# Kernel optimization log

Hardware: AMD Instinct MI355X
Metric: run time of the kernel (lower is better)

The kernel has to match this reference:

```python
import jax, jax.numpy as jnp
import numpy as np

N = 199968   # active voxels (flat tokens)
W = 3125     # number of windows
S = 64       # window capacity
D = 128      # d_model
H = 8        # nhead
DH = D // H
DFF = 256


def layer_norm(x, g, b, eps=1e-5):
    m = x.mean(-1, keepdims=True)
    v = ((x - m) ** 2).mean(-1, keepdims=True)
    return (x - m) / jnp.sqrt(v + eps) * g + b


def setup_inputs() -> dict:
    key = jax.random.key(0)
    ks = jax.random.split(key, 12)
    s = 0.02
    src = jax.random.normal(ks[0], (N, D), dtype=jnp.float32)
    pos = jax.random.normal(ks[1], (W, S, D), dtype=jnp.float32)
    # token i occupies flat window-slot i; slots >= N are padding
    inds = jnp.arange(N, dtype=jnp.int64)
    key_padding_mask = (jnp.arange(W * S) >= N).reshape(W, S)  # True = pad
    in_proj_w = jax.random.normal(ks[2], (3 * D, D), dtype=jnp.float32) * s
    in_proj_b = jax.random.normal(ks[3], (3 * D,), dtype=jnp.float32) * s
    out_w = jax.random.normal(ks[4], (D, D), dtype=jnp.float32) * s
    out_b = jax.random.normal(ks[5], (D,), dtype=jnp.float32) * s
    w1 = jax.random.normal(ks[6], (DFF, D), dtype=jnp.float32) * s
    b1 = jax.random.normal(ks[7], (DFF,), dtype=jnp.float32) * s
    w2 = jax.random.normal(ks[8], (D, DFF), dtype=jnp.float32) * s
    b2 = jax.random.normal(ks[9], (D,), dtype=jnp.float32) * s
    ln1_g = jnp.ones((D,), jnp.float32); ln1_b = jnp.zeros((D,), jnp.float32)
    ln2_g = jnp.ones((D,), jnp.float32); ln2_b = jnp.zeros((D,), jnp.float32)
    return {"src": src, "pos": pos, "inds": inds,
            "key_padding_mask": key_padding_mask,
            "in_proj_w": in_proj_w, "in_proj_b": in_proj_b,
            "out_w": out_w, "out_b": out_b,
            "w1": w1, "b1": b1, "w2": w2, "b2": b2,
            "ln1_g": ln1_g, "ln1_b": ln1_b, "ln2_g": ln2_g, "ln2_b": ln2_b}


def reference(src, pos, inds, key_padding_mask, in_proj_w, in_proj_b,
              out_w, out_b, w1, b1, w2, b2, ln1_g, ln1_b, ln2_g, ln2_b):
    # ---- flat2window_v2: scatter flat tokens into window slots ----
    win = jnp.zeros((W * S, D), src.dtype).at[inds].set(src).reshape(W, S, D)
    # q = k = feat + pos, v = feat (post-norm, self-attention branch)
    qk_in = win + pos
    Wq, Wk, Wv = in_proj_w[:D], in_proj_w[D:2 * D], in_proj_w[2 * D:]
    bq, bk, bv = in_proj_b[:D], in_proj_b[D:2 * D], in_proj_b[2 * D:]
    q = (qk_in @ Wq.T + bq).reshape(W, S, H, DH)
    k = (qk_in @ Wk.T + bk).reshape(W, S, H, DH)
    v = (win @ Wv.T + bv).reshape(W, S, H, DH)
    scale = 1.0 / jnp.sqrt(jnp.asarray(DH, src.dtype))
    scores = jnp.einsum('wqhd,wkhd->whqk', q, k) * scale  # [W,H,S,S]
    scores = jnp.where(key_padding_mask[:, None, None, :], -jnp.inf, scores)
    attn = jax.nn.softmax(scores, axis=-1)
    o = jnp.einsum('whqk,wkhd->wqhd', attn, v).reshape(W, S, D)
    o = o @ out_w.T + out_b
    # ---- window2flat_v2: gather back to flat tokens ----
    att_out = o.reshape(W * S, D)[inds]
    # ---- residual + LN + FFN + LN (post_norm=True, dropout=0 eval) ----
    x = layer_norm(src + att_out, ln1_g, ln1_b)
    ffn = jax.nn.relu(x @ w1.T + b1) @ w2.T + b2
    x = layer_norm(x + ffn, ln2_g, ln2_b)
    return x
```

## Files before the change

### kernel.cpp

```cpp
#include <hip/hip_runtime.h>
#include <stdint.h>

typedef __attribute__((ext_vector_type(8))) short bf16x8;
typedef __attribute__((ext_vector_type(4))) float f32x4;
typedef __attribute__((ext_vector_type(16))) float f32x16;

#define MFMA16(a,b,c) __builtin_amdgcn_mfma_f32_16x16x32_bf16((a),(b),(c),0,0,0)
#define MFMA32(a,b,c) __builtin_amdgcn_mfma_f32_32x32x16_bf16((a),(b),(c),0,0,0)

#define RA 0
#define RB 16384
#define RC 32768
#define RED 49152
#define LDSB (49152 + 2048)
#define QSCALE 0.36067376022224085f

static __device__ __forceinline__ int swz16(int row, int byte){ return byte ^ ((row&15)<<4); }
static __device__ __forceinline__ int swz8 (int row, int byte){ return byte ^ ((row&7)<<4); }

static __device__ __forceinline__ void barrier_lds(){
  asm volatile("s_waitcnt lgkmcnt(0)" ::: "memory");
  __builtin_amdgcn_s_barrier();
}

static __device__ __forceinline__ uint32_t cvtpk(float lo, float hi){
  uint32_t r; asm("v_cvt_pk_bf16_f32 %0, %1, %2" : "=v"(r) : "v"(lo), "v"(hi)); return r;
}
static __device__ __forceinline__ unsigned short f2bf(float f){
  union { float f; uint32_t u; } c; c.f = f;
  return (unsigned short)((c.u + 0x7fffu + ((c.u >> 16) & 1u)) >> 16);
}
static __device__ __forceinline__ f32x16 zero16(){
  f32x16 z;
  #pragma unroll
  for (int e=0;e<16;++e) z[e]=0.f;
  return z;
}

static __device__ __forceinline__ void packPT(const f32x16 s, int hi, bf16x8& fA, bf16x8& fB){
  uint32_t PA0=cvtpk(s[0],s[1]),  PA1=cvtpk(s[2],s[3]);
  uint32_t PB0=cvtpk(s[4],s[5]),  PB1=cvtpk(s[6],s[7]);
  uint32_t PC0=cvtpk(s[8],s[9]),  PC1=cvtpk(s[10],s[11]);
  uint32_t PD0=cvtpk(s[12],s[13]),PD1=cvtpk(s[14],s[15]);
  uint32_t x0 = __shfl_xor(hi ? PA0 : PB0, 32);
  uint32_t x1 = __shfl_xor(hi ? PA1 : PB1, 32);
  uint32_t y0 = __shfl_xor(hi ? PC0 : PD0, 32);
  uint32_t y1 = __shfl_xor(hi ? PC1 : PD1, 32);
  union { uint32_t u[4]; bf16x8 v; } ua, ub;
  ua.u[0] = hi ? x0 : PA0;  ua.u[1] = hi ? x1 : PA1;
  ua.u[2] = hi ? PB0 : x0;  ua.u[3] = hi ? PB1 : x1;
  ub.u[0] = hi ? y0 : PC0;  ub.u[1] = hi ? y1 : PC1;
  ub.u[2] = hi ? PD0 : y0;  ub.u[3] = hi ? PD1 : y1;
  fA = ua.v; fB = ub.v;
}

__global__ void convert_weights(const float* __restrict__ ipw, const float* __restrict__ ow,
                                const float* __restrict__ w1, const float* __restrict__ w2,
                                unsigned short* __restrict__ wsb){
  int i = blockIdx.x*256 + threadIdx.x;
  if (i >= 131072) return;
  const float* sp; int m, K, KC;
  if (i < 49152)      { sp = ipw; m = i;         K=128; KC=4; }
  else if (i < 65536) { sp = ow;  m = i - 49152; K=128; KC=4; }
  else if (i < 98304) { sp = w1;  m = i - 65536; K=128; KC=4; }
  else                { sp = w2;  m = i - 98304; K=256; KC=8; }
  int e  = m & 7;
  int L  = (m >> 3) & 63;
  int b  = m >> 9;
  int kc = b % KC;
  int Mt = b / KC;
  float v = sp[(Mt*16 + (L&15))*K + kc*32 + (L>>4)*8 + e];
  if (i < 16384) v *= QSCALE;
  wsb[i] = f2bf(v);
}

__global__ __launch_bounds__(256, 3) void enc_kernel(
    const float* __restrict__ src, const float* __restrict__ pos,
    const float* __restrict__ ipb, const float* __restrict__ obp,
    const float* __restrict__ b1p, const float* __restrict__ b2p,
    const float* __restrict__ g1p, const float* __restrict__ be1p,
    const float* __restrict__ g2p, const float* __restrict__ be2p,
    const unsigned short* __restrict__ wb,
    float* __restrict__ out, int nTok)
{
  __shared__ __align__(16) char sm[LDSB];
  const int win  = blockIdx.x;
  const int tid  = threadIdx.x;
  const int lane = tid & 63;
  const int wid  = tid >> 6;
  const int l15  = lane & 15;
  const int lg   = lane >> 4;
  const int l31  = lane & 31;
  const int hi   = lane >> 5;
  const f32x4 FZ = {0.f,0.f,0.f,0.f};
  const int colbase = wid*32;
  const unsigned short* wlane = wb + lane*8;
  const int valid = nTok - win*64;

  f32x4 srcv[2][4];
  #pragma unroll
  for (int Mtl=0;Mtl<2;++Mtl){
    #pragma unroll
    for (int g=0;g<4;++g){
      int row  = g*16 + l15;
      int grow = win*64 + row;
      int col  = colbase + Mtl*16 + lg*4;
      f32x4 sv = FZ;
      if (grow < nTok) sv = *(const f32x4*)(src + (size_t)grow*128 + col);
      f32x4 pv = *(const f32x4*)(pos + (size_t)win*8192 + row*128 + col);
      srcv[Mtl][g] = sv;
      uint2 wv, qv;
      wv.x = cvtpk(sv[0], sv[1]);             wv.y = cvtpk(sv[2], sv[3]);
      qv.x = cvtpk(sv[0]+pv[0], sv[1]+pv[1]); qv.y = cvtpk(sv[2]+pv[2], sv[3]+pv[3]);
      int cb = col*2;
      *(uint2*)(sm + RA + row*256 + swz16(row, cb)) = qv;
      *(uint2*)(sm + RB + row*256 + swz16(row, cb)) = wv;
    }
  }
  barrier_lds();

  {
    {
      bf16x8 wv8[8];
      #pragma unroll
      for (int i=0;i<8;++i)
        wv8[i] = *(const bf16x8*)(wlane + (size_t)(((16 + wid*2 + (i>>2))*4 + (i&3)) << 9));
      f32x4 vacc[2][4];
      #pragma unroll
      for (int Mtl=0;Mtl<2;++Mtl){
        #pragma unroll
        for (int g=0;g<4;++g) vacc[Mtl][g] = FZ;
      }
      #pragma unroll
      for (int kc=0;kc<4;++kc){
        bf16x8 aw[4];
        #pragma unroll
        for (int g=0;g<4;++g){
          int r2 = g*16 + l15;
          aw[g] = *(const bf16x8*)(sm + RB + r2*256 + swz16(r2, kc*64 + lg*16));
        }
        #pragma unroll
        for (int Mtl=0;Mtl<2;++Mtl){
          #pragma unroll
          for (int g=0;g<4;++g) vacc[Mtl][g] = MFMA16(aw[g], wv8[Mtl*4+kc], vacc[Mtl][g]);
        }
      }
      #pragma unroll
      for (int Mtl=0;Mtl<2;++Mtl){
        int d = colbase + Mtl*16 + l15;
        float bv = ipb[256 + d];
        #pragma unroll
        for (int g=0;g<4;++g){
          uint2 vp;
          vp.x = cvtpk(vacc[Mtl][g][0]+bv, vacc[Mtl][g][1]+bv);
          vp.y = cvtpk(vacc[Mtl][g][2]+bv, vacc[Mtl][g][3]+bv);
          *(uint2*)(sm + RC + d*128 + swz8(d, (g*16 + lg*4)*2)) = vp;
        }
      }
    }

    f32x4 qacc[2][4];
    {
      bf16x8 wq8[8];
      #pragma unroll
      for (int i=0;i<8;++i)
        wq8[i] = *(const bf16x8*)(wlane + (size_t)((( 0 + wid*2 + (i>>2))*4 + (i&3)) << 9));
      #pragma unroll
      for (int Mtl=0;Mtl<2;++Mtl){
        #pragma unroll
        for (int g=0;g<4;++g) qacc[Mtl][g]=FZ;
      }
      #pragma unroll
      for (int kc=0;kc<4;++kc){
        bf16x8 bq[4];
        #pragma unroll
        for (int g=0;g<4;++g){
          int r2 = g*16 + l15;
          bq[g] = *(const bf16x8*)(sm + RA + r2*256 + swz16(r2, kc*64 + lg*16));
        }
        #pragma unroll
        for (int Mtl=0;Mtl<2;++Mtl){
          #pragma unroll
          for (int g=0;g<4;++g) qacc[Mtl][g] = MFMA16(wq8[Mtl*4+kc], bq[g], qacc[Mtl][g]);
        }
      }
    }
    barrier_lds();

    #pragma unroll
    for (int Mtl=0;Mtl<2;++Mtl){
      f32x4 qb4 = *(const f32x4*)(ipb + colbase + Mtl*16 + lg*4);
      #pragma unroll
      for (int g=0;g<4;++g){
        int tok = g*16 + l15;
        int cb  = (colbase + Mtl*16 + lg*4)*2;
        uint2 qp;
        qp.x = cvtpk(qacc[Mtl][g][0]+qb4[0]*QSCALE, qacc[Mtl][g][1]+qb4[1]*QSCALE);
        qp.y = cvtpk(qacc[Mtl][g][2]+qb4[2]*QSCALE, qacc[Mtl][g][3]+qb4[3]*QSCALE);
        *(uint2*)(sm + RB + tok*256 + swz16(tok, cb)) = qp;
      }
    }

    f32x4 kacc[2][4];
    {
      bf16x8 wk8[8];
      #pragma unroll
      for (int i=0;i<8;++i)
        wk8[i] = *(const bf16x8*)(wlane + (size_t)((( 8 + wid*2 + (i>>2))*4 + (i&3)) << 9));
      #pragma unroll
      for (int Mtl=0;Mtl<2;++Mtl){
        #pragma unroll
        for (int g=0;g<4;++g) kacc[Mtl][g]=FZ;
      }
      #pragma unroll
      for (int kc=0;kc<4;++kc){
        bf16x8 bq[4];
        #pragma unroll
        for (int g=0;g<4;++g){
          int r2 = g*16 + l15;
          bq[g] = *(const bf16x8*)(sm + RA + r2*256 + swz16(r2, kc*64 + lg*16));
        }
        #pragma unroll
        for (int Mtl=0;Mtl<2;++Mtl){
          #pragma unroll
          for (int g=0;g<4;++g) kacc[Mtl][g] = MFMA16(wk8[Mtl*4+kc], bq[g], kacc[Mtl][g]);
        }
      }
    }
    barrier_lds();

    #pragma unroll
    for (int Mtl=0;Mtl<2;++Mtl){
      f32x4 kb4 = *(const f32x4*)(ipb + 128 + colbase + Mtl*16 + lg*4);
      #pragma unroll
      for (int g=0;g<4;++g){
        int tok = g*16 + l15;
        int cb  = (colbase + Mtl*16 + lg*4)*2;
        uint2 kp;
        kp.x = cvtpk(kacc[Mtl][g][0]+kb4[0], kacc[Mtl][g][1]+kb4[1]);
        kp.y = cvtpk(kacc[Mtl][g][2]+kb4[2], kacc[Mtl][g][3]+kb4[3]);
        *(uint2*)(sm + RA + tok*256 + swz16(tok, cb)) = kp;
      }
    }
  }

  #pragma unroll
  for (int hh=0; hh<2; ++hh){
    const int head = wid*2 + hh;
    bf16x8 ka0 = *(const bf16x8*)(sm + RA + (     l31)*256 + swz16(l31,    head*32 + hi*16));
    bf16x8 ka1 = *(const bf16x8*)(sm + RA + (32 + l31)*256 + swz16(32+l31, head*32 + hi*16));
    #pragma unroll
    for (int qt=0; qt<2; ++qt){
      int qrow = qt*32 + l31;
      bf16x8 qb = *(const bf16x8*)(sm + RB + qrow*256 + swz16(qrow, head*32 + hi*16));
      f32x16 s0 = MFMA32(ka0, qb, zero16());
      f32x16 s1 = MFMA32(ka1, qb, zero16());
      if (valid < 64){
        #pragma unroll
        for (int e=0;e<16;++e){
          int kk = (e&3) + 8*(e>>2) + 4*hi;
          if (kk      >= valid) s0[e] = -1e30f;
          if (kk + 32 >= valid) s1[e] = -1e30f;
        }
      }
      #pragma unroll
      for (int e=0;e<16;++e) s0[e] = __builtin_amdgcn_exp2f(s0[e]);
      #pragma unroll
      for (int e=0;e<16;++e) s1[e] = __builtin_amdgcn_exp2f(s1[e]);
      float t[8];
      #pragma unroll
      for (int e=0;e<8;++e) t[e] = (s0[2*e]+s0[2*e+1]) + (s1[2*e]+s1[2*e+1]);
      float u0 = t[0]+t[1], u1 = t[2]+t[3], u2 = t[4]+t[5], u3 = t[6]+t[7];
      float sum = (u0+u1)+(u2+u3);
      sum += __shfl_xor(sum, 32);
      float rden = __builtin_amdgcn_rcpf(sum);

      bf16x8 fr[4];
      packPT(s0, hi, fr[0], fr[1]);
      packPT(s1, hi, fr[2], fr[3]);
      f32x16 oacc = zero16();
      #pragma unroll
      for (int kc=0;kc<4;++kc){
        int vrow = head*16 + l15;
        bf16x8 va = *(const bf16x8*)(sm + RC + vrow*128 + swz8(vrow, kc*32 + hi*16));
        oacc = MFMA32(va, fr[kc], oacc);
      }
      int tok = qt*32 + l31;
      uint2 o01, o23;
      o01.x = cvtpk(oacc[0]*rden, oacc[1]*rden);
      o01.y = cvtpk(oacc[2]*rden, oacc[3]*rden);
      o23.x = cvtpk(oacc[4]*rden, oacc[5]*rden);
      o23.y = cvtpk(oacc[6]*rden, oacc[7]*rden);
      *(uint2*)(sm + RB + tok*256 + swz16(tok, (head*16 + 4*hi)*2))     = o01;
      *(uint2*)(sm + RB + tok*256 + swz16(tok, (head*16 + 8 + 4*hi)*2)) = o23;
    }
  }
  barrier_lds();

  f32x4 xva[2][4];
  {
    bf16x8 wo8[8];
    #pragma unroll
    for (int i=0;i<8;++i)
      wo8[i] = *(const bf16x8*)(wlane + 49152 + (size_t)(((wid*2 + (i>>2))*4 + (i&3)) << 9));
    f32x4 oa[2][4];
    #pragma unroll
    for (int Mtl=0;Mtl<2;++Mtl){
      #pragma unroll
      for (int g=0;g<4;++g) oa[Mtl][g] = FZ;
    }
    #pragma unroll
    for (int kc=0;kc<4;++kc){
      bf16x8 bo[4];
      #pragma unroll
      for (int g=0;g<4;++g){
        int r2 = g*16 + l15;
        bo[g] = *(const bf16x8*)(sm + RB + r2*256 + swz16(r2, kc*64 + lg*16));
      }
      #pragma unroll
      for (int Mtl=0;Mtl<2;++Mtl){
        #pragma unroll
        for (int g=0;g<4;++g) oa[Mtl][g] = MFMA16(wo8[Mtl*4+kc], bo[g], oa[Mtl][g]);
      }
    }
    #pragma unroll
    for (int Mtl=0;Mtl<2;++Mtl){
      f32x4 ob4 = *(const f32x4*)(obp + colbase + Mtl*16 + lg*4);
      #pragma unroll
      for (int g=0;g<4;++g){
        #pragma unroll
        for (int r=0;r<4;++r) xva[Mtl][g][r] = oa[Mtl][g][r] + ob4[r] + srcv[Mtl][g][r];
      }
    }
    float* redc = (float*)(sm + RED);
    #pragma unroll
    for (int g=0;g<4;++g){
      float ts=0.f, tq=0.f;
      #pragma unroll
      for (int Mtl=0;Mtl<2;++Mtl){
        #pragma unroll
        for (int r=0;r<4;++r){ float v = xva[Mtl][g][r]; ts += v; tq += v*v; }
      }
      ts += __shfl_xor(ts,16); tq += __shfl_xor(tq,16);
      ts += __shfl_xor(ts,32); tq += __shfl_xor(tq,32);
      if (lg == 0) *(float2*)(redc + (g*16+l15)*8 + wid*2) = make_float2(ts, tq);
    }
    barrier_lds();
    float mean4[4], rstd4[4];
    #pragma unroll
    for (int g=0;g<4;++g){
      int tok = g*16 + l15;
      f32x4 ra = *(const f32x4*)(redc + tok*8);
      f32x4 rb = *(const f32x4*)(redc + tok*8 + 4);
      float sum = ra[0]+ra[2]+rb[0]+rb[2];
      float sq  = ra[1]+ra[3]+rb[1]+rb[3];
      mean4[g] = sum*(1.f/128.f);
      rstd4[g] = __builtin_amdgcn_rsqf(sq*(1.f/128.f) - mean4[g]*mean4[g] + 1e-5f);
    }
    #pragma unroll
    for (int Mtl=0;Mtl<2;++Mtl){
      f32x4 g4 = *(const f32x4*)(g1p  + colbase + Mtl*16 + lg*4);
      f32x4 e4 = *(const f32x4*)(be1p + colbase + Mtl*16 + lg*4);
      #pragma unroll
      for (int g=0;g<4;++g){
        int tok = g*16 + l15;
        int cb  = (colbase + Mtl*16 + lg*4)*2;
        #pragma unroll
        for (int r=0;r<4;++r) xva[Mtl][g][r] = (xva[Mtl][g][r]-mean4[g])*rstd4[g]*g4[r] + e4[r];
        uint2 xp;
        xp.x = cvtpk(xva[Mtl][g][0], xva[Mtl][g][1]);
        xp.y = cvtpk(xva[Mtl][g][2], xva[Mtl][g][3]);
        *(uint2*)(sm + RA + tok*256 + swz16(tok, cb)) = xp;
      }
    }
  }
  barrier_lds();

  {
    char* hreg = (wid < 2) ? (sm + RB) : (sm + RC);
    int   hoff = (wid & 1)*64;
    #pragma unroll 1
    for (int half=0; half<2; ++half){
      bf16x8 wf[8];
      #pragma unroll
      for (int i=0;i<8;++i)
        wf[i] = *(const bf16x8*)(wlane + 65536 + (size_t)(((wid*4 + half*2 + (i>>2))*4 + (i&3)) << 9));
      f32x4 ha[2][4];
      #pragma unroll
      for (int Mtl=0;Mtl<2;++Mtl){
        #pragma unroll
        for (int g=0;g<4;++g) ha[Mtl][g] = FZ;
      }
      #pragma unroll
      for (int kc=0;kc<4;++kc){
        bf16x8 bx[4];
        #pragma unroll
        for (int g=0;g<4;++g){
          int r2 = g*16 + l15;
          bx[g] = *(const bf16x8*)(sm + RA + r2*256 + swz16(r2, kc*64 + lg*16));
        }
        #pragma unroll
        for (int Mtl=0;Mtl<2;++Mtl){
          #pragma unroll
          for (int g=0;g<4;++g) ha[Mtl][g] = MFMA16(wf[Mtl*4+kc], bx[g], ha[Mtl][g]);
        }
      }
      #pragma unroll
      for (int Mtl=0;Mtl<2;++Mtl){
        int Mg = half*2 + Mtl;
        f32x4 b14 = *(const f32x4*)(b1p + wid*64 + Mg*16 + lg*4);
        #pragma unroll
        for (int g=0;g<4;++g){
          int tok = g*16 + l15;
          float h0 = fmaxf(ha[Mtl][g][0]+b14[0], 0.f);
          float h1 = fmaxf(ha[Mtl][g][1]+b14[1], 0.f);
          float h2 = fmaxf(ha[Mtl][g][2]+b14[2], 0.f);
          float h3 = fmaxf(ha[Mtl][g][3]+b14[3], 0.f);
          int cb = (hoff + Mg*16 + lg*4)*2;
          uint2 hp;
          hp.x = cvtpk(h0, h1);
          hp.y = cvtpk(h2, h3);
          *(uint2*)(hreg + tok*256 + swz16(tok, cb)) = hp;
        }
      }
    }
  }
  barrier_lds();

  {
    f32x4 fa[2][4];
    #pragma unroll
    for (int Mtl=0;Mtl<2;++Mtl){
      #pragma unroll
      for (int g=0;g<4;++g) fa[Mtl][g] = FZ;
    }
    #pragma unroll 1
    for (int half=0; half<2; ++half){
      bf16x8 wg[8];
      #pragma unroll
      for (int i=0;i<8;++i)
        wg[i] = *(const bf16x8*)(wlane + 98304 + (size_t)(((wid*2 + (i>>2))*8 + half*4 + (i&3)) << 9));
      const char* hsrc = sm + (half ? RC : RB);
      #pragma unroll
      for (int kc=0;kc<4;++kc){
        bf16x8 bh[4];
        #pragma unroll
        for (int g=0;g<4;++g){
          int r2 = g*16 + l15;
          bh[g] = *(const bf16x8*)(hsrc + r2*256 + swz16(r2, kc*64 + lg*16));
        }
        #pragma unroll
        for (int Mtl=0;Mtl<2;++Mtl){
          #pragma unroll
          for (int g=0;g<4;++g) fa[Mtl][g] = MFMA16(wg[Mtl*4+kc], bh[g], fa[Mtl][g]);
        }
      }
    }
    #pragma unroll
    for (int Mtl=0;Mtl<2;++Mtl){
      f32x4 b24 = *(const f32x4*)(b2p + colbase + Mtl*16 + lg*4);
      #pragma unroll
      for (int g=0;g<4;++g){
        #pragma unroll
        for (int r=0;r<4;++r) fa[Mtl][g][r] += b24[r] + xva[Mtl][g][r];
      }
    }
    float* redc = (float*)(sm + RED);
    #pragma unroll
    for (int g=0;g<4;++g){
      float ts=0.f, tq=0.f;
      #pragma unroll
      for (int Mtl=0;Mtl<2;++Mtl){
        #pragma unroll
        for (int r=0;r<4;++r){ float v = fa[Mtl][g][r]; ts += v; tq += v*v; }
      }
      ts += __shfl_xor(ts,16); tq += __shfl_xor(tq,16);
      ts += __shfl_xor(ts,32); tq += __shfl_xor(tq,32);
      if (lg == 0) *(float2*)(redc + (g*16+l15)*8 + wid*2) = make_float2(ts, tq);
    }
    barrier_lds();
    float m2[4], r2v[4];
    #pragma unroll
    for (int g=0;g<4;++g){
      int tok = g*16 + l15;
      f32x4 ra = *(const f32x4*)(redc + tok*8);
      f32x4 rb = *(const f32x4*)(redc + tok*8 + 4);
      float sum = ra[0]+ra[2]+rb[0]+rb[2];
      float sq  = ra[1]+ra[3]+rb[1]+rb[3];
      m2[g]  = sum*(1.f/128.f);
      r2v[g] = __builtin_amdgcn_rsqf(sq*(1.f/128.f) - m2[g]*m2[g] + 1e-5f);
    }
    #pragma unroll
    for (int Mtl=0;Mtl<2;++Mtl){
      f32x4 g4 = *(const f32x4*)(g2p  + colbase + Mtl*16 + lg*4);
      f32x4 e4 = *(const f32x4*)(be2p + colbase + Mtl*16 + lg*4);
      #pragma unroll
      for (int g=0;g<4;++g){
        int tok = g*16 + l15;
        f32x4 o4;
        #pragma unroll
        for (int r=0;r<4;++r) o4[r] = (fa[Mtl][g][r]-m2[g])*r2v[g]*g4[r] + e4[r];
        int X = ((colbase + Mtl*16 + lg*4)*4) ^ (l15<<4);
        *(f32x4*)(sm + ((tok<32)? RA : RB) + (tok&31)*512 + X) = o4;
      }
    }
    barrier_lds();
    #pragma unroll
    for (int j=0;j<8;++j){
      int row  = wid*16 + j*2 + hi;
      int grow = win*64 + row;
      if (grow < nTok){
        int X = (l31*16) ^ ((row&15)<<4);
        f32x4 v = *(const f32x4*)(sm + ((row<32)? RA : RB) + (row&31)*512 + X);
        *(f32x4*)(out + (size_t)grow*128 + l31*4) = v;
      }
    }
  }
}

extern "C" void kernel_launch(void* const* d_in, const int* in_sizes, int n_in,
                              void* d_out, int out_size, void* d_ws, size_t ws_size,
                              hipStream_t stream) {
  const float* src = (const float*)d_in[0];
  const float* pos = (const float*)d_in[1];
  const float* ipw = (const float*)d_in[4];
  const float* ipb = (const float*)d_in[5];
  const float* ow  = (const float*)d_in[6];
  const float* ob  = (const float*)d_in[7];
  const float* w1  = (const float*)d_in[8];
  const float* b1  = (const float*)d_in[9];
  const float* w2  = (const float*)d_in[10];
  const float* b2  = (const float*)d_in[11];
  const float* g1  = (const float*)d_in[12];
  const float* be1 = (const float*)d_in[13];
  const float* g2  = (const float*)d_in[14];
  const float* be2 = (const float*)d_in[15];
  int nTok = in_sizes[0] / 128;
  int nWin = in_sizes[1] / 8192;
  unsigned short* wsb = (unsigned short*)d_ws;

  hipLaunchKernelGGL(convert_weights, dim3(512), dim3(256), 0, stream, ipw, ow, w1, w2, wsb);
  hipLaunchKernelGGL(enc_kernel, dim3(nWin), dim3(256), 0, stream,
                     src, pos, ipb, ob, b1, b2, g1, be1, g2, be2, wsb,
                     (float*)d_out, nTok);
}
```

Before: 139.9 us.

## Split per-window work across 8 waves instead of 4

The block grows from 256 to 512 threads, so each wave owns 16 output columns and one attention head rather than 32 columns and two heads. This halves the per-wave accumulator and weight-register arrays, raising the launch-bounds occupancy target from 3 to 4 blocks per CU. The LayerNorm reduction scratch is widened to hold eight partial sums per token, and the FFN hidden-layer write offsets are remapped to match. More waves per window add barrier contention, and each wave reuses its LDS operand loads across fewer MFMAs.

```diff
diff --git a/kernel.cpp b/kernel.cpp
--- a/kernel.cpp
+++ b/kernel.cpp
@@ -12,7 +12,7 @@
 #define RB 16384
 #define RC 32768
 #define RED 49152
-#define LDSB (49152 + 2048)
+#define LDSB (49152 + 4096)
 #define QSCALE 0.36067376022224085f
 
 static __device__ __forceinline__ int swz16(int row, int byte){ return byte ^ ((row&15)<<4); }
@@ -74,7 +74,7 @@
   wsb[i] = f2bf(v);
 }
 
-__global__ __launch_bounds__(256, 3) void enc_kernel(
+__global__ __launch_bounds__(512, 4) void enc_kernel(
     const float* __restrict__ src, const float* __restrict__ pos,
     const float* __restrict__ ipb, const float* __restrict__ obp,
     const float* __restrict__ b1p, const float* __restrict__ b2p,
@@ -93,44 +93,38 @@
   const int l31  = lane & 31;
   const int hi   = lane >> 5;
   const f32x4 FZ = {0.f,0.f,0.f,0.f};
-  const int colbase = wid*32;
+  const int colbase = wid*16;
   const unsigned short* wlane = wb + lane*8;
   const int valid = nTok - win*64;
 
-  f32x4 srcv[2][4];
+  f32x4 srcv[4];
   #pragma unroll
-  for (int Mtl=0;Mtl<2;++Mtl){
-    #pragma unroll
-    for (int g=0;g<4;++g){
-      int row  = g*16 + l15;
-      int grow = win*64 + row;
-      int col  = colbase + Mtl*16 + lg*4;
-      f32x4 sv = FZ;
-      if (grow < nTok) sv = *(const f32x4*)(src + (size_t)grow*128 + col);
-      f32x4 pv = *(const f32x4*)(pos + (size_t)win*8192 + row*128 + col);
-      srcv[Mtl][g] = sv;
-      uint2 wv, qv;
-      wv.x = cvtpk(sv[0], sv[1]);             wv.y = cvtpk(sv[2], sv[3]);
-      qv.x = cvtpk(sv[0]+pv[0], sv[1]+pv[1]); qv.y = cvtpk(sv[2]+pv[2], sv[3]+pv[3]);
-      int cb = col*2;
-      *(uint2*)(sm + RA + row*256 + swz16(row, cb)) = qv;
-      *(uint2*)(sm + RB + row*256 + swz16(row, cb)) = wv;
-    }
+  for (int g=0;g<4;++g){
+    int row  = g*16 + l15;
+    int grow = win*64 + row;
+    int col  = colbase + lg*4;
+    f32x4 sv = FZ;
+    if (grow < nTok) sv = *(const f32x4*)(src + (size_t)grow*128 + col);
+    f32x4 pv = *(const f32x4*)(pos + (size_t)win*8192 + row*128 + col);
+    srcv[g] = sv;
+    uint2 wv, qv;
+    wv.x = cvtpk(sv[0], sv[1]);             wv.y = cvtpk(sv[2], sv[3]);
+    qv.x = cvtpk(sv[0]+pv[0], sv[1]+pv[1]); qv.y = cvtpk(sv[2]+pv[2], sv[3]+pv[3]);
+    int cb = col*2;
+    *(uint2*)(sm + RA + row*256 + swz16(row, cb)) = qv;
+    *(uint2*)(sm + RB + row*256 + swz16(row, cb)) = wv;
   }
   barrier_lds();
 
   {
     {
-      bf16x8 wv8[8];
-      #pragma unroll
-      for (int i=0;i<8;++i)
-        wv8[i] = *(const bf16x8*)(wlane + (size_t)(((16 + wid*2 + (i>>2))*4 + (i&3)) << 9));
-      f32x4 vacc[2][4];
-      #pragma unroll
-      for (int Mtl=0;Mtl<2;++Mtl){
-        #pragma unroll
-        for (int g=0;g<4;++g) vacc[Mtl][g] = FZ;
-      }
+      bf16x8 wv8[4];
+      #pragma unroll
+      for (int kc=0;kc<4;++kc)
+        wv8[kc] = *(const bf16x8*)(wlane + (size_t)(((16 + wid)*4 + kc) << 9));
+      f32x4 vacc[4];
+      #pragma unroll
+      for (int g=0;g<4;++g) vacc[g] = FZ;
       #pragma unroll
       for (int kc=0;kc<4;++kc){
         bf16x8 aw[4];
@@ -140,36 +134,27 @@
           aw[g] = *(const bf16x8*)(sm + RB + r2*256 + swz16(r2, kc*64 + lg*16));
         }
         #pragma unroll
-        for (int Mtl=0;Mtl<2;++Mtl){
-          #pragma unroll
-          for (int g=0;g<4;++g) vacc[Mtl][g] = MFMA16(aw[g], wv8[Mtl*4+kc], vacc[Mtl][g]);
-        }
-      }
-      #pragma unroll
-      for (int Mtl=0;Mtl<2;++Mtl){
-        int d = colbase + Mtl*16 + l15;
-        float bv = ipb[256 + d];
-        #pragma unroll
-        for (int g=0;g<4;++g){
-          uint2 vp;
-          vp.x = cvtpk(vacc[Mtl][g][0]+bv, vacc[Mtl][g][1]+bv);
-          vp.y = cvtpk(vacc[Mtl][g][2]+bv, vacc[Mtl][g][3]+bv);
-          *(uint2*)(sm + RC + d*128 + swz8(d, (g*16 + lg*4)*2)) = vp;
-        }
-      }
-    }
-
-    f32x4 qacc[2][4];
+        for (int g=0;g<4;++g) vacc[g] = MFMA16(aw[g], wv8[kc], vacc[g]);
+      }
+      int d = colbase + l15;
+      float bv = ipb[256 + d];
+      #pragma unroll
+      for (int g=0;g<4;++g){
+        uint2 vp;
+        vp.x = cvtpk(vacc[g][0]+bv, vacc[g][1]+bv);
+        vp.y = cvtpk(vacc[g][2]+bv, vacc[g][3]+bv);
+        *(uint2*)(sm + RC + d*128 + swz8(d, (g*16 + lg*4)*2)) = vp;
+      }
+    }
+
+    f32x4 qacc[4];
     {
-      bf16x8 wq8[8];
-      #pragma unroll
-      for (int i=0;i<8;++i)
-        wq8[i] = *(const bf16x8*)(wlane + (size_t)((( 0 + wid*2 + (i>>2))*4 + (i&3)) << 9));
-      #pragma unroll
-      for (int Mtl=0;Mtl<2;++Mtl){
-        #pragma unroll
-        for (int g=0;g<4;++g) qacc[Mtl][g]=FZ;
-      }
+      bf16x8 wq8[4];
+      #pragma unroll
+      for (int kc=0;kc<4;++kc)
+        wq8[kc] = *(const bf16x8*)(wlane + (size_t)((wid*4 + kc) << 9));
+      #pragma unroll
+      for (int g=0;g<4;++g) qacc[g]=FZ;
       #pragma unroll
       for (int kc=0;kc<4;++kc){
         bf16x8 bq[4];
@@ -179,39 +164,32 @@
           bq[g] = *(const bf16x8*)(sm + RA + r2*256 + swz16(r2, kc*64 + lg*16));
         }
         #pragma unroll
-        for (int Mtl=0;Mtl<2;++Mtl){
-          #pragma unroll
-          for (int g=0;g<4;++g) qacc[Mtl][g] = MFMA16(wq8[Mtl*4+kc], bq[g], qacc[Mtl][g]);
-        }
+        for (int g=0;g<4;++g) qacc[g] = MFMA16(wq8[kc], bq[g], qacc[g]);
       }
     }
     barrier_lds();
 
-    #pragma unroll
-    for (int Mtl=0;Mtl<2;++Mtl){
-      f32x4 qb4 = *(const f32x4*)(ipb + colbase + Mtl*16 + lg*4);
+    {
+      f32x4 qb4 = *(const f32x4*)(ipb + colbase + lg*4);
       #pragma unroll
       for (int g=0;g<4;++g){
         int tok = g*16 + l15;
-        int cb  = (colbase + Mtl*16 + lg*4)*2;
+        int cb  = (colbase + lg*4)*2;
         uint2 qp;
-        qp.x = cvtpk(qacc[Mtl][g][0]+qb4[0]*QSCALE, qacc[Mtl][g][1]+qb4[1]*QSCALE);
-        qp.y = cvtpk(qacc[Mtl][g][2]+qb4[2]*QSCALE, qacc[Mtl][g][3]+qb4[3]*QSCALE);
+        qp.x = cvtpk(qacc[g][0]+qb4[0]*QSCALE, qacc[g][1]+qb4[1]*QSCALE);
+        qp.y = cvtpk(qacc[g][2]+qb4[2]*QSCALE, qacc[g][3]+qb4[3]*QSCALE);
         *(uint2*)(sm + RB + tok*256 + swz16(tok, cb)) = qp;
       }
     }
 
-    f32x4 kacc[2][4];
+    f32x4 kacc[4];
     {
-      bf16x8 wk8[8];
-      #pragma unroll
-      for (int i=0;i<8;++i)
-        wk8[i] = *(const bf16x8*)(wlane + (size_t)((( 8 + wid*2 + (i>>2))*4 + (i&3)) << 9));
-      #pragma unroll
-      for (int Mtl=0;Mtl<2;++Mtl){
-        #pragma unroll
-        for (int g=0;g<4;++g) kacc[Mtl][g]=FZ;
-      }
+      bf16x8 wk8[4];
+      #pragma unroll
+      for (int kc=0;kc<4;++kc)
+        wk8[kc] = *(const bf16x8*)(wlane + (size_t)(((8 + wid)*4 + kc) << 9));
+      #pragma unroll
+      for (int g=0;g<4;++g) kacc[g]=FZ;
       #pragma unroll
       for (int kc=0;kc<4;++kc){
         bf16x8 bq[4];
@@ -221,32 +199,27 @@
           bq[g] = *(const bf16x8*)(sm + RA + r2*256 + swz16(r2, kc*64 + lg*16));
         }
         #pragma unroll
-        for (int Mtl=0;Mtl<2;++Mtl){
-          #pragma unroll
-          for (int g=0;g<4;++g) kacc[Mtl][g] = MFMA16(wk8[Mtl*4+kc], bq[g], kacc[Mtl][g]);
-        }
+        for (int g=0;g<4;++g) kacc[g] = MFMA16(wk8[kc], bq[g], kacc[g]);
       }
     }
     barrier_lds();
 
-    #pragma unroll
-    for (int Mtl=0;Mtl<2;++Mtl){
-      f32x4 kb4 = *(const f32x4*)(ipb + 128 + colbase + Mtl*16 + lg*4);
+    {
+      f32x4 kb4 = *(const f32x4*)(ipb + 128 + colbase + lg*4);
       #pragma unroll
       for (int g=0;g<4;++g){
         int tok = g*16 + l15;
-        int cb  = (colbase + Mtl*16 + lg*4)*2;
+        int cb  = (colbase + lg*4)*2;
         uint2 kp;
-        kp.x = cvtpk(kacc[Mtl][g][0]+kb4[0], kacc[Mtl][g][1]+kb4[1]);
-        kp.y = cvtpk(kacc[Mtl][g][2]+kb4[2], kacc[Mtl][g][3]+kb4[3]);
+        kp.x = cvtpk(kacc[g][0]+kb4[0], kacc[g][1]+kb4[1]);
+        kp.y = cvtpk(kacc[g][2]+kb4[2], kacc[g][3]+kb4[3]);
         *(uint2*)(sm + RA + tok*256 + swz16(tok, cb)) = kp;
       }
     }
   }
 
-  #pragma unroll
-  for (int hh=0; hh<2; ++hh){
-    const int head = wid*2 + hh;
+  {
+    const int head = wid;
     bf16x8 ka0 = *(const bf16x8*)(sm + RA + (     l31)*256 + swz16(l31,    head*32 + hi*16));
     bf16x8 ka1 = *(const bf16x8*)(sm + RA + (32 + l31)*256 + swz16(32+l31, head*32 + hi*16));
     #pragma unroll
@@ -297,18 +270,16 @@
   }
   barrier_lds();
 
-  f32x4 xva[2][4];
+  f32x4 xva[4];
+  float mean4[4], rstd4[4];
   {
-    bf16x8 wo8[8];
-    #pragma unroll
-    for (int i=0;i<8;++i)
-      wo8[i] = *(const bf16x8*)(wlane + 49152 + (size_t)(((wid*2 + (i>>2))*4 + (i&3)) << 9));
-    f32x4 oa[2][4];
-    #pragma unroll
-    for (int Mtl=0;Mtl<2;++Mtl){
-      #pragma unroll
-      for (int g=0;g<4;++g) oa[Mtl][g] = FZ;
-    }
+    bf16x8 wo8[4];
+    #pragma unroll
+    for (int kc=0;kc<4;++kc)
+      wo8[kc] = *(const bf16x8*)(wlane + 49152 + (size_t)((wid*4 + kc) << 9));
+    f32x4 oa[4];
+    #pragma unroll
+    for (int g=0;g<4;++g) oa[g] = FZ;
     #pragma unroll
     for (int kc=0;kc<4;++kc){
       bf16x8 bo[4];
@@ -318,79 +289,64 @@
         bo[g] = *(const bf16x8*)(sm + RB + r2*256 + swz16(r2, kc*64 + lg*16));
       }
       #pragma unroll
-      for (int Mtl=0;Mtl<2;++Mtl){
-        #pragma unroll
-        for (int g=0;g<4;++g) oa[Mtl][g] = MFMA16(wo8[Mtl*4+kc], bo[g], oa[Mtl][g]);
-      }
-    }
-    #pragma unroll
-    for (int Mtl=0;Mtl<2;++Mtl){
-      f32x4 ob4 = *(const f32x4*)(obp + colbase + Mtl*16 + lg*4);
-      #pragma unroll
-      for (int g=0;g<4;++g){
-        #pragma unroll
-        for (int r=0;r<4;++r) xva[Mtl][g][r] = oa[Mtl][g][r] + ob4[r] + srcv[Mtl][g][r];
-      }
+      for (int g=0;g<4;++g) oa[g] = MFMA16(wo8[kc], bo[g], oa[g]);
+    }
+    f32x4 ob4 = *(const f32x4*)(obp + colbase + lg*4);
+    #pragma unroll
+    for (int g=0;g<4;++g){
+      #pragma unroll
+      for (int r=0;r<4;++r) xva[g][r] = oa[g][r] + ob4[r] + srcv[g][r];
     }
     float* redc = (float*)(sm + RED);
     #pragma unroll
     for (int g=0;g<4;++g){
-      float ts=0.f, tq=0.f;
-      #pragma unroll
-      for (int Mtl=0;Mtl<2;++Mtl){
-        #pragma unroll
-        for (int r=0;r<4;++r){ float v = xva[Mtl][g][r]; ts += v; tq += v*v; }
-      }
+      float ts = xva[g][0]+xva[g][1]+xva[g][2]+xva[g][3];
+      float tq = xva[g][0]*xva[g][0]+xva[g][1]*xva[g][1]+xva[g][2]*xva[g][2]+xva[g][3]*xva[g][3];
       ts += __shfl_xor(ts,16); tq += __shfl_xor(tq,16);
       ts += __shfl_xor(ts,32); tq += __shfl_xor(tq,32);
-      if (lg == 0) *(float2*)(redc + (g*16+l15)*8 + wid*2) = make_float2(ts, tq);
+      if (lg == 0) *(float2*)(redc + (g*16+l15)*16 + wid*2) = make_float2(ts, tq);
     }
     barrier_lds();
-    float mean4[4], rstd4[4];
     #pragma unroll
     for (int g=0;g<4;++g){
       int tok = g*16 + l15;
-      f32x4 ra = *(const f32x4*)(redc + tok*8);
-      f32x4 rb = *(const f32x4*)(redc + tok*8 + 4);
-      float sum = ra[0]+ra[2]+rb[0]+rb[2];
-      float sq  = ra[1]+ra[3]+rb[1]+rb[3];
+      float sum=0.f, sq=0.f;
+      #pragma unroll
+      for (int c=0;c<4;++c){
+        f32x4 rr = *(const f32x4*)(redc + tok*16 + c*4);
+        sum += rr[0]+rr[2];
+        sq  += rr[1]+rr[3];
+      }
       mean4[g] = sum*(1.f/128.f);
       rstd4[g] = __builtin_amdgcn_rsqf(sq*(1.f/128.f) - mean4[g]*mean4[g] + 1e-5f);
     }
-    #pragma unroll
-    for (int Mtl=0;Mtl<2;++Mtl){
-      f32x4 g4 = *(const f32x4*)(g1p  + colbase + Mtl*16 + lg*4);
-      f32x4 e4 = *(const f32x4*)(be1p + colbase + Mtl*16 + lg*4);
-      #pragma unroll
-      for (int g=0;g<4;++g){
-        int tok = g*16 + l15;
-        int cb  = (colbase + Mtl*16 + lg*4)*2;
-        #pragma unroll
-        for (int r=0;r<4;++r) xva[Mtl][g][r] = (xva[Mtl][g][r]-mean4[g])*rstd4[g]*g4[r] + e4[r];
-        uint2 xp;
-        xp.x = cvtpk(xva[Mtl][g][0], xva[Mtl][g][1]);
-        xp.y = cvtpk(xva[Mtl][g][2], xva[Mtl][g][3]);
-        *(uint2*)(sm + RA + tok*256 + swz16(tok, cb)) = xp;
-      }
+    f32x4 g4 = *(const f32x4*)(g1p  + colbase + lg*4);
+    f32x4 e4 = *(const f32x4*)(be1p + colbase + lg*4);
+    #pragma unroll
+    for (int g=0;g<4;++g){
+      int tok = g*16 + l15;
+      int cb  = (colbase + lg*4)*2;
+      #pragma unroll
+      for (int r=0;r<4;++r) xva[g][r] = (xva[g][r]-mean4[g])*rstd4[g]*g4[r] + e4[r];
+      uint2 xp;
+      xp.x = cvtpk(xva[g][0], xva[g][1]);
+      xp.y = cvtpk(xva[g][2], xva[g][3]);
+      *(uint2*)(sm + RA + tok*256 + swz16(tok, cb)) = xp;
     }
   }
   barrier_lds();
 
   {
-    char* hreg = (wid < 2) ? (sm + RB) : (sm + RC);
-    int   hoff = (wid & 1)*64;
+    char* hreg = (wid < 4) ? (sm + RB) : (sm + RC);
     #pragma unroll 1
     for (int half=0; half<2; ++half){
-      bf16x8 wf[8];
-      #pragma unroll
-      for (int i=0;i<8;++i)
-        wf[i] = *(const bf16x8*)(wlane + 65536 + (size_t)(((wid*4 + half*2 + (i>>2))*4 + (i&3)) << 9));
-      f32x4 ha[2][4];
-      #pragma unroll
-      for (int Mtl=0;Mtl<2;++Mtl){
-        #pragma unroll
-        for (int g=0;g<4;++g) ha[Mtl][g] = FZ;
-      }
+      bf16x8 wf[4];
+      #pragma unroll
+      for (int kc=0;kc<4;++kc)
+        wf[kc] = *(const bf16x8*)(wlane + 65536 + (size_t)(((wid*2 + half)*4 + kc) << 9));
+      f32x4 ha[4];
+      #pragma unroll
+      for (int g=0;g<4;++g) ha[g] = FZ;
       #pragma unroll
       for (int kc=0;kc<4;++kc){
         bf16x8 bx[4];
@@ -400,114 +356,94 @@
           bx[g] = *(const bf16x8*)(sm + RA + r2*256 + swz16(r2, kc*64 + lg*16));
         }
         #pragma unroll
-        for (int Mtl=0;Mtl<2;++Mtl){
-          #pragma unroll
-          for (int g=0;g<4;++g) ha[Mtl][g] = MFMA16(wf[Mtl*4+kc], bx[g], ha[Mtl][g]);
-        }
-      }
-      #pragma unroll
-      for (int Mtl=0;Mtl<2;++Mtl){
-        int Mg = half*2 + Mtl;
-        f32x4 b14 = *(const f32x4*)(b1p + wid*64 + Mg*16 + lg*4);
-        #pragma unroll
-        for (int g=0;g<4;++g){
-          int tok = g*16 + l15;
-          float h0 = fmaxf(ha[Mtl][g][0]+b14[0], 0.f);
-          float h1 = fmaxf(ha[Mtl][g][1]+b14[1], 0.f);
-          float h2 = fmaxf(ha[Mtl][g][2]+b14[2], 0.f);
-          float h3 = fmaxf(ha[Mtl][g][3]+b14[3], 0.f);
-          int cb = (hoff + Mg*16 + lg*4)*2;
-          uint2 hp;
-          hp.x = cvtpk(h0, h1);
-          hp.y = cvtpk(h2, h3);
-          *(uint2*)(hreg + tok*256 + swz16(tok, cb)) = hp;
-        }
+        for (int g=0;g<4;++g) ha[g] = MFMA16(wf[kc], bx[g], ha[g]);
+      }
+      f32x4 b14 = *(const f32x4*)(b1p + (wid*2+half)*16 + lg*4);
+      #pragma unroll
+      for (int g=0;g<4;++g){
+        int tok = g*16 + l15;
+        float h0 = fmaxf(ha[g][0]+b14[0], 0.f);
+        float h1 = fmaxf(ha[g][1]+b14[1], 0.f);
+        float h2 = fmaxf(ha[g][2]+b14[2], 0.f);
+        float h3 = fmaxf(ha[g][3]+b14[3], 0.f);
+        int cb = ((wid&3)*32 + half*16 + lg*4)*2;
+        uint2 hp;
+        hp.x = cvtpk(h0, h1);
+        hp.y = cvtpk(h2, h3);
+        *(uint2*)(hreg + tok*256 + swz16(tok, cb)) = hp;
       }
     }
   }
   barrier_lds();
 
   {
-    f32x4 fa[2][4];
-    #pragma unroll
-    for (int Mtl=0;Mtl<2;++Mtl){
-      #pragma unroll
-      for (int g=0;g<4;++g) fa[Mtl][g] = FZ;
-    }
+    f32x4 fa[4];
+    #pragma unroll
+    for (int g=0;g<4;++g) fa[g] = FZ;
     #pragma unroll 1
     for (int half=0; half<2; ++half){
-      bf16x8 wg[8];
-      #pragma unroll
-      for (int i=0;i<8;++i)
-        wg[i] = *(const bf16x8*)(wlane + 98304 + (size_t)(((wid*2 + (i>>2))*8 + half*4 + (i&3)) << 9));
+      bf16x8 wg[4];
+      #pragma unroll
+      for (int kcl=0;kcl<4;++kcl)
+        wg[kcl] = *(const bf16x8*)(wlane + 98304 + (size_t)((wid*8 + half*4 + kcl) << 9));
       const char* hsrc = sm + (half ? RC : RB);
       #pragma unroll
-      for (int kc=0;kc<4;++kc){
+      for (int kcl=0;kcl<4;++kcl){
         bf16x8 bh[4];
         #pragma unroll
         for (int g=0;g<4;++g){
           int r2 = g*16 + l15;
-          bh[g] = *(const bf16x8*)(hsrc + r2*256 + swz16(r2, kc*64 + lg*16));
-        }
-        #pragma unroll
-        for (int Mtl=0;Mtl<2;++Mtl){
-          #pragma unroll
-          for (int g=0;g<4;++g) fa[Mtl][g] = MFMA16(wg[Mtl*4+kc], bh[g], fa[Mtl][g]);
-        }
-      }
-    }
-    #pragma unroll
-    for (int Mtl=0;Mtl<2;++Mtl){
-      f32x4 b24 = *(const f32x4*)(b2p + colbase + Mtl*16 + lg*4);
-      #pragma unroll
-      for (int g=0;g<4;++g){
-        #pragma unroll
-        for (int r=0;r<4;++r) fa[Mtl][g][r] += b24[r] + xva[Mtl][g][r];
-      }
+          bh[g] = *(const bf16x8*)(hsrc + r2*256 + swz16(r2, kcl*64 + lg*16));
+        }
+        #pragma unroll
+        for (int g=0;g<4;++g) fa[g] = MFMA16(wg[kcl], bh[g], fa[g]);
+      }
+    }
+    f32x4 b24 = *(const f32x4*)(b2p + colbase + lg*4);
+    #pragma unroll
+    for (int g=0;g<4;++g){
+      #pragma unroll
+      for (int r=0;r<4;++r) fa[g][r] += b24[r] + xva[g][r];
     }
     float* redc = (float*)(sm + RED);
     #pragma unroll
     for (int g=0;g<4;++g){
-      float ts=0.f, tq=0.f;
-      #pragma unroll
-      for (int Mtl=0;Mtl<2;++Mtl){
-        #pragma unroll
-        for (int r=0;r<4;++r){ float v = fa[Mtl][g][r]; ts += v; tq += v*v; }
-      }
+      float ts = fa[g][0]+fa[g][1]+fa[g][2]+fa[g][3];
+      float tq = fa[g][0]*fa[g][0]+fa[g][1]*fa[g][1]+fa[g][2]*fa[g][2]+fa[g][3]*fa[g][3];
       ts += __shfl_xor(ts,16); tq += __shfl_xor(tq,16);
       ts += __shfl_xor(ts,32); tq += __shfl_xor(tq,32);
-      if (lg == 0) *(float2*)(redc + (g*16+l15)*8 + wid*2) = make_float2(ts, tq);
+      if (lg == 0) *(float2*)(redc + (g*16+l15)*16 + wid*2) = make_float2(ts, tq);
     }
     barrier_lds();
     float m2[4], r2v[4];
     #pragma unroll
     for (int g=0;g<4;++g){
       int tok = g*16 + l15;
-      f32x4 ra = *(const f32x4*)(redc + tok*8);
-      f32x4 rb = *(const f32x4*)(redc + tok*8 + 4);
-      float sum = ra[0]+ra[2]+rb[0]+rb[2];
-      float sq  = ra[1]+ra[3]+rb[1]+rb[3];
+      float sum=0.f, sq=0.f;
+      #pragma unroll
+      for (int c=0;c<4;++c){
+        f32x4 rr = *(const f32x4*)(redc + tok*16 + c*4);
+        sum += rr[0]+rr[2];
+        sq  += rr[1]+rr[3];
+      }
       m2[g]  = sum*(1.f/128.f);
       r2v[g] = __builtin_amdgcn_rsqf(sq*(1.f/128.f) - m2[g]*m2[g] + 1e-5f);
     }
-    #pragma unroll
-    for (int Mtl=0;Mtl<2;++Mtl){
-      f32x4 g4 = *(const f32x4*)(g2p  + colbase + Mtl*16 + lg*4);
-      f32x4 e4 = *(const f32x4*)(be2p + colbase + Mtl*16 + lg*4);
-      #pragma unroll
-      for (int g=0;g<4;++g){
-        int tok = g*16 + l15;
-        f32x4 o4;
-        #pragma unroll
-        for (int r=0;r<4;++r) o4[r] = (fa[Mtl][g][r]-m2[g])*r2v[g]*g4[r] + e4[r];
-        int X = ((colbase + Mtl*16 + lg*4)*4) ^ (l15<<4);
-        *(f32x4*)(sm + ((tok<32)? RA : RB) + (tok&31)*512 + X) = o4;
-      }
+    f32x4 g4 = *(const f32x4*)(g2p  + colbase + lg*4);
+    f32x4 e4 = *(const f32x4*)(be2p + colbase + lg*4);
+    #pragma unroll
+    for (int g=0;g<4;++g){
+      int tok = g*16 + l15;
+      f32x4 o4;
+      #pragma unroll
+      for (int r=0;r<4;++r) o4[r] = (fa[g][r]-m2[g])*r2v[g]*g4[r] + e4[r];
+      int X = ((colbase + lg*4)*4) ^ (l15<<4);
+      *(f32x4*)(sm + ((tok<32)? RA : RB) + (tok&31)*512 + X) = o4;
     }
     barrier_lds();
     #pragma unroll
-    for (int j=0;j<8;++j){
-      int row  = wid*16 + j*2 + hi;
+    for (int j=0;j<4;++j){
+      int row  = wid*8 + j*2 + hi;
       int grow = win*64 + row;
       if (grow < nTok){
         int X = (l31*16) ^ ((row&15)<<4);
@@ -540,7 +476,7 @@
   unsigned short* wsb = (unsigned short*)d_ws;
 
   hipLaunchKernelGGL(convert_weights, dim3(512), dim3(256), 0, stream, ipw, ow, w1, w2, wsb);
-  hipLaunchKernelGGL(enc_kernel, dim3(nWin), dim3(256), 0, stream,
+  hipLaunchKernelGGL(enc_kernel, dim3(nWin), dim3(512), 0, stream,
                      src, pos, ipb, ob, b1, b2, g1, be1, g2, be2, wsb,
                      (float*)d_out, nTok);
 }
```

Result: slower. 159.7 us (+14.1%).
